# Kernel tuning notes

Measured on AMD Instinct MI355X. Metric: run time of the kernel, lower is better.

Reference implementation:

```python
import jax, jax.numpy as jnp
import numpy as np

MAXLEN = 100  # target_node_incoming_edge_maxlim in to_dense_batch_JY


def setup_inputs() -> dict:
    key = jax.random.key(0)
    ks = jax.random.split(key, 6)
    N, F, H, B = 500000, 64, 64, 8192
    x = jax.random.normal(ks[0], (N, F), dtype=jnp.float32)
    index = jnp.sort(jax.random.randint(ks[1], (N,), 0, B)).astype(jnp.int64)
    s = 1.0 / np.sqrt(H)  # torch LSTM reset_parameters: U(-1/sqrt(H), 1/sqrt(H))
    W_ih = jax.random.uniform(ks[2], (4 * H, F), jnp.float32, -s, s)
    W_hh = jax.random.uniform(ks[3], (4 * H, H), jnp.float32, -s, s)
    b_ih = jax.random.uniform(ks[4], (4 * H,), jnp.float32, -s, s)
    b_hh = jax.random.uniform(ks[5], (4 * H,), jnp.float32, -s, s)
    return {"x": x, "W_ih": W_ih, "W_hh": W_hh, "b_ih": b_ih, "b_hh": b_hh,
            "index": index, "dim_size": B}


def _lstm_last_hidden(dense, mask, W_ih, W_hh, b_ih, b_hh):
    """Run a single-layer LSTM over dense [B,L,F]; freeze state where mask is
    False, which reproduces pack_sequence semantics (ht = hidden at last valid
    step of each sequence; zero-length sequences stay at h0=0)."""
    B, L, F = dense.shape
    H = W_hh.shape[1]
    # input projection for all timesteps at once: [B, L, 4H]
    xg = jnp.einsum('blf,gf->blg', dense, W_ih) + (b_ih + b_hh)

    def step(carry, inp):
        h, c = carry
        g_x, m = inp                      # g_x: [B,4H], m: [B] bool
        g = g_x + h @ W_hh.T
        i, f, gc, o = jnp.split(g, 4, axis=-1)  # torch gate order: i, f, g, o
        i = jax.nn.sigmoid(i)
        f = jax.nn.sigmoid(f)
        gc = jnp.tanh(gc)
        o = jax.nn.sigmoid(o)
        c_new = f * c + i * gc
        h_new = o * jnp.tanh(c_new)
        m2 = m[:, None]
        return (jnp.where(m2, h_new, h), jnp.where(m2, c_new, c)), None

    h0 = jnp.zeros((B, H), dense.dtype)
    (h, _c), _ = jax.lax.scan(step, (h0, h0),
                              (jnp.swapaxes(xg, 0, 1), mask.T))
    return h  # [B, H] == ht[-1]


def reference(x, W_ih, W_hh, b_ih, b_hh, index, dim_size):
    N, F = x.shape
    index = index.astype(jnp.int32)
    # per-graph node counts and exclusive-cumsum offsets (index is sorted)
    counts = jax.ops.segment_sum(jnp.ones(N, jnp.int32), index,
                                 num_segments=dim_size)
    offsets = jnp.concatenate([jnp.zeros(1, jnp.int32),
                               jnp.cumsum(counts)[:-1].astype(jnp.int32)])
    pos = jnp.arange(N, dtype=jnp.int32) - offsets[index]  # position in graph
    valid = pos < MAXLEN                                   # truncate to 100
    # scatter into dense [B, MAXLEN, F]; invalid rows are zeroed and added at
    # slot 0 so they are no-ops
    dense = jnp.zeros((dim_size, MAXLEN, F), x.dtype)
    dense = dense.at[index, jnp.where(valid, pos, 0)].add(
        jnp.where(valid[:, None], x, 0.0))
    seq_len = jnp.minimum(counts, MAXLEN)
    mask = jnp.arange(MAXLEN)[None, :] < seq_len[:, None]  # [B, MAXLEN]
    return _lstm_last_hidden(dense, mask, W_ih, W_hh, b_ih, b_hh)
```

## Files before the change

kernel.cpp:

```cpp
#include <hip/hip_runtime.h>

#define MAXLEN 100
#define HDIM 64
#define CH 4
#define NSEG 12
#define SROW 72
#define SPLANE (CH * SROW + 8)
#define HSTR 72
#define L2E 1.44269504f

typedef __attribute__((ext_vector_type(8))) short bf16x8;
typedef __attribute__((ext_vector_type(4))) float f32x4;

#define LGKM_BARRIER() asm volatile("s_waitcnt lgkmcnt(0)\n\ts_barrier" ::: "memory")

__device__ __forceinline__ unsigned short f2bf_u(float f) {
    unsigned u = __float_as_uint(f);
    u += 0x7fffu + ((u >> 16) & 1u);
    return (unsigned short)(u >> 16);
}
__device__ __forceinline__ unsigned pk2(float a, float b) {
    return (unsigned)f2bf_u(a) | ((unsigned)f2bf_u(b) << 16);
}
__device__ __forceinline__ bf16x8 pack8(f32x4 a, f32x4 b) {
    union { unsigned u[4]; bf16x8 v; } c;
    c.u[0] = pk2(a[0], a[1]); c.u[1] = pk2(a[2], a[3]);
    c.u[2] = pk2(b[0], b[1]); c.u[3] = pk2(b[2], b[3]);
    return c.v;
}
__device__ __forceinline__ float sig_b(float v, float bs) {
    return __builtin_amdgcn_rcpf(1.0f + __builtin_amdgcn_exp2f(fmaf(v, -L2E, bs)));
}
__device__ __forceinline__ float tanh_b(float v, float bs2) {
    return fmaf(2.0f, __builtin_amdgcn_rcpf(1.0f + __builtin_amdgcn_exp2f(fmaf(v, -2.0f * L2E, bs2))), -1.0f);
}
__device__ __forceinline__ float tanh_p(float v) {
    return fmaf(2.0f, __builtin_amdgcn_rcpf(1.0f + __builtin_amdgcn_exp2f(v * (-2.0f * L2E))), -1.0f);
}

__global__ __launch_bounds__(256, 3)
void lstm12_kernel(const float* __restrict__ x,
                   const float* __restrict__ Wih,
                   const float* __restrict__ Whh,
                   const float* __restrict__ bih,
                   const float* __restrict__ bhh,
                   const int* __restrict__ index,
                   float* __restrict__ out, int N, int B) {
    const int tid  = threadIdx.x;
    const int w    = tid >> 6;
    const int lane = tid & 63;
    const int l15  = lane & 15;
    const int quad = lane >> 4;
    const int segbase = blockIdx.x * NSEG;
    const int ncol = w * 16 + l15;

    __shared__ __align__(16) unsigned short xst[NSEG * SPLANE];
    __shared__ __align__(16) unsigned short hst[2][16][HSTR];
    __shared__ int sstart[NSEG], slen[NSEG];

    if (tid < NSEG) {
        const int b = segbase + tid;
        int s = 0, len = 0;
        if (b < B) {
            int lo = 0, hi = N;
            while (lo < hi) { int m = (lo + hi) >> 1; if (index[m] < b) lo = m + 1; else hi = m; }
            s = lo;
            hi = N;
            while (lo < hi) { int m = (lo + hi) >> 1; if (index[m] < b + 1) lo = m + 1; else hi = m; }
            len = lo - s;
            len = len < MAXLEN ? len : MAXLEN;
        }
        sstart[tid] = s;
        slen[tid] = len;
    }
    for (int i = tid; i < 2 * 16 * HSTR / 2; i += 256) ((int*)hst)[i] = 0;
    __syncthreads();

    bf16x8 wi[4][2], wh[4][2];
    float bs[4];
#pragma unroll
    for (int g = 0; g < 4; ++g) {
        const int row = g * HDIM + ncol;
        const float bb = bih[row] + bhh[row];
        bs[g] = (g == 2) ? (-2.0f * L2E) * bb : (-L2E) * bb;
#pragma unroll
        for (int kt = 0; kt < 2; ++kt) {
            const f32x4* pi = (const f32x4*)(Wih + (size_t)row * HDIM + kt * 32 + quad * 8);
            const f32x4* ph = (const f32x4*)(Whh + (size_t)row * HDIM + kt * 32 + quad * 8);
            wi[g][kt] = pack8(pi[0], pi[1]);
            wh[g][kt] = pack8(ph[0], ph[1]);
        }
    }

    int len3[3];
#pragma unroll
    for (int r = 0; r < 3; ++r) len3[r] = slen[quad * 3 + r];
    int lmax = 0;
#pragma unroll
    for (int i = 0; i < NSEG; ++i) { int v = slen[i]; lmax = v > lmax ? v : lmax; }
    lmax = __builtin_amdgcn_readfirstlane(lmax);

    const int sS = tid >> 4, sT = (tid >> 2) & 3, sC = tid & 3;
    const int sst = (tid < 192) ? sstart[sS] : 0;
    const int sln = (tid < 192) ? slen[sS] : 0;

    f32x4 pre[4];

#define ISSUE(t0_)                                                              \
    if (w < 3) {                                                                \
        int ct = (t0_) + sT;                                                    \
        ct = (sln > 0) ? (ct < sln ? ct : sln - 1) : 0;                         \
        int row = sst + ct;                                                     \
        row = row < N - 1 ? row : N - 1;                                        \
        const f32x4* p_ = (const f32x4*)(x + (size_t)row * HDIM + sC * 16);     \
        pre[0] = p_[0]; pre[1] = p_[1]; pre[2] = p_[2]; pre[3] = p_[3];         \
    }
#define COMMIT()                                                                \
    if (w < 3) {                                                                \
        uint4 o1, o2;                                                           \
        o1.x = pk2(pre[0][0], pre[0][1]); o1.y = pk2(pre[0][2], pre[0][3]);     \
        o1.z = pk2(pre[1][0], pre[1][1]); o1.w = pk2(pre[1][2], pre[1][3]);     \
        o2.x = pk2(pre[2][0], pre[2][1]); o2.y = pk2(pre[2][2], pre[2][3]);     \
        o2.z = pk2(pre[3][0], pre[3][1]); o2.w = pk2(pre[3][2], pre[3][3]);     \
        unsigned short* d_ = &xst[sS * SPLANE + sT * SROW + sC * 16];           \
        *(uint4*)d_ = o1; *(uint4*)(d_ + 8) = o2;                               \
    }

    const int m3 = l15 & 3;
    const int xp = (l15 >> 2) * 3 + (m3 < 2 ? m3 : 2);
    const unsigned short* xb = &xst[xp * SPLANE + quad * 8];

    f32x4 accx[4];
#define ACCX(tt_)                                                               \
    {                                                                           \
        const unsigned short* xr_ = xb + (tt_) * SROW;                          \
        bf16x8 xa0_ = *(const bf16x8*)(xr_);                                    \
        bf16x8 xa1_ = *(const bf16x8*)(xr_ + 32);                               \
        _Pragma("unroll")                                                       \
        for (int g_ = 0; g_ < 4; ++g_) {                                        \
            f32x4 a_ = __builtin_amdgcn_mfma_f32_16x16x32_bf16(xa0_, wi[g_][0], cz, 0, 0, 0); \
            accx[g_] = __builtin_amdgcn_mfma_f32_16x16x32_bf16(xa1_, wi[g_][1], a_, 0, 0, 0); \
        }                                                                       \
    }

    float c3[3] = {0, 0, 0}, h3[3] = {0, 0, 0};
    const f32x4 cz = {0.0f, 0.0f, 0.0f, 0.0f};
    const int nch = (lmax + CH - 1) / CH;

    if (nch > 0) {
        ISSUE(0);
        COMMIT();
        LGKM_BARRIER();
        ACCX(0);
        if (nch > 1) ISSUE(CH);

        for (int ch = 0; ch < nch; ++ch) {
            const int t0 = ch * CH;
#pragma unroll
            for (int tt = 0; tt < CH; ++tt) {
                const int t = t0 + tt;
                const int pb = tt & 1, nb = pb ^ 1;

                const unsigned short* hr = &hst[pb][l15][quad * 8];
                bf16x8 ha0 = *(const bf16x8*)(hr);
                bf16x8 ha1 = *(const bf16x8*)(hr + 32);

                f32x4 acc[4];
#pragma unroll
                for (int g = 0; g < 4; ++g) {
                    f32x4 a = __builtin_amdgcn_mfma_f32_16x16x32_bf16(ha0, wh[g][0], accx[g], 0, 0, 0);
                    acc[g] = __builtin_amdgcn_mfma_f32_16x16x32_bf16(ha1, wh[g][1], a, 0, 0, 0);
                }

                if (tt + 1 < CH) ACCX(tt + 1);

#pragma unroll
                for (int r = 0; r < 3; ++r) {
                    float gi = sig_b (acc[0][r], bs[0]);
                    float gf = sig_b (acc[1][r], bs[1]);
                    float gg = tanh_b(acc[2][r], bs[2]);
                    float go = sig_b (acc[3][r], bs[3]);
                    float cn = fmaf(gf, c3[r], gi * gg);
                    float hn = go * tanh_p(cn);
                    const bool up = t < len3[r];
                    c3[r] = up ? cn : c3[r];
                    h3[r] = up ? hn : h3[r];
                    hst[nb][quad * 4 + r][ncol] = f2bf_u(h3[r]);
                }
                LGKM_BARRIER();
            }
            if (ch + 1 < nch) {
                COMMIT();
                LGKM_BARRIER();
                ACCX(0);
                if (ch + 2 < nch) ISSUE((ch + 2) * CH);
            }
        }
    }

#pragma unroll
    for (int r = 0; r < 3; ++r) {
        const int seg = segbase + quad * 3 + r;
        if (seg < B) out[(size_t)seg * HDIM + ncol] = h3[r];
    }
#undef ISSUE
#undef COMMIT
#undef ACCX
}

extern "C" void kernel_launch(void* const* d_in, const int* in_sizes, int n_in,
                              void* d_out, int out_size, void* d_ws, size_t ws_size,
                              hipStream_t stream) {
    const float* x     = (const float*)d_in[0];
    const float* Wih   = (const float*)d_in[1];
    const float* Whh   = (const float*)d_in[2];
    const float* bih   = (const float*)d_in[3];
    const float* bhh   = (const float*)d_in[4];
    const int*   index = (const int*)d_in[5];

    const int N = in_sizes[5];
    const int B = out_size / HDIM;

    const int nblocks = (B + NSEG - 1) / NSEG;
    lstm12_kernel<<<nblocks, 256, 0, stream>>>(x, Wih, Whh, bih, bhh, index,
                                               (float*)d_out, N, B);
}
```

Baseline: 251.5 us.

## Run each LSTM group in a single wave with all weights in registers

Replaces the 256-thread, 12-segment block with a single 64-lane wave that handles 8 segments and holds all four gate column tiles of W_ih and W_hh in registers. This removes the cross-wave barriers and the LDS staging of x, since x rows are loaded straight into registers two steps ahead. The gate scale factors are folded into the weights, the bias seeds the MFMA accumulator, and bf16 conversion uses the hardware v_cvt_pk_bf16_f32 instruction. In exchange each wave does four times the MFMA work per step on a serial dependency chain, register pressure rises sharply, and the MFMA tiles use only 8 of their 16 rows.

```diff
diff --git a/kernel.cpp b/kernel.cpp
--- a/kernel.cpp
+++ b/kernel.cpp
@@ -2,210 +2,163 @@
 
 #define MAXLEN 100
 #define HDIM 64
-#define CH 4
-#define NSEG 12
-#define SROW 72
-#define SPLANE (CH * SROW + 8)
+#define SEGW 8
 #define HSTR 72
 #define L2E 1.44269504f
 
 typedef __attribute__((ext_vector_type(8))) short bf16x8;
 typedef __attribute__((ext_vector_type(4))) float f32x4;
 
-#define LGKM_BARRIER() asm volatile("s_waitcnt lgkmcnt(0)\n\ts_barrier" ::: "memory")
-
-__device__ __forceinline__ unsigned short f2bf_u(float f) {
-    unsigned u = __float_as_uint(f);
-    u += 0x7fffu + ((u >> 16) & 1u);
-    return (unsigned short)(u >> 16);
-}
-__device__ __forceinline__ unsigned pk2(float a, float b) {
-    return (unsigned)f2bf_u(a) | ((unsigned)f2bf_u(b) << 16);
+__device__ __forceinline__ unsigned cvtpk(float a, float b) {
+    unsigned r;
+    asm("v_cvt_pk_bf16_f32 %0, %1, %2" : "=v"(r) : "v"(a), "v"(b));
+    return r;
 }
 __device__ __forceinline__ bf16x8 pack8(f32x4 a, f32x4 b) {
     union { unsigned u[4]; bf16x8 v; } c;
-    c.u[0] = pk2(a[0], a[1]); c.u[1] = pk2(a[2], a[3]);
-    c.u[2] = pk2(b[0], b[1]); c.u[3] = pk2(b[2], b[3]);
+    c.u[0] = cvtpk(a[0], a[1]); c.u[1] = cvtpk(a[2], a[3]);
+    c.u[2] = cvtpk(b[0], b[1]); c.u[3] = cvtpk(b[2], b[3]);
     return c.v;
 }
-__device__ __forceinline__ float sig_b(float v, float bs) {
-    return __builtin_amdgcn_rcpf(1.0f + __builtin_amdgcn_exp2f(fmaf(v, -L2E, bs)));
+__device__ __forceinline__ float sig_pre(float a) {
+    return __builtin_amdgcn_rcpf(1.0f + __builtin_amdgcn_exp2f(a));
 }
-__device__ __forceinline__ float tanh_b(float v, float bs2) {
-    return fmaf(2.0f, __builtin_amdgcn_rcpf(1.0f + __builtin_amdgcn_exp2f(fmaf(v, -2.0f * L2E, bs2))), -1.0f);
+__device__ __forceinline__ float tanh_pre(float a) {
+    return fmaf(2.0f, __builtin_amdgcn_rcpf(1.0f + __builtin_amdgcn_exp2f(a)), -1.0f);
 }
 __device__ __forceinline__ float tanh_p(float v) {
     return fmaf(2.0f, __builtin_amdgcn_rcpf(1.0f + __builtin_amdgcn_exp2f(v * (-2.0f * L2E))), -1.0f);
 }
 
-__global__ __launch_bounds__(256, 3)
-void lstm12_kernel(const float* __restrict__ x,
-                   const float* __restrict__ Wih,
-                   const float* __restrict__ Whh,
-                   const float* __restrict__ bih,
-                   const float* __restrict__ bhh,
-                   const int* __restrict__ index,
-                   float* __restrict__ out, int N, int B) {
-    const int tid  = threadIdx.x;
-    const int w    = tid >> 6;
-    const int lane = tid & 63;
+__global__ __launch_bounds__(64, 1)
+void lstm_wave_kernel(const float* __restrict__ x,
+                      const float* __restrict__ Wih,
+                      const float* __restrict__ Whh,
+                      const float* __restrict__ bih,
+                      const float* __restrict__ bhh,
+                      const int* __restrict__ index,
+                      float* __restrict__ out, int N, int B) {
+    const int lane = threadIdx.x;
     const int l15  = lane & 15;
     const int quad = lane >> 4;
-    const int segbase = blockIdx.x * NSEG;
-    const int ncol = w * 16 + l15;
+    const int segbase = blockIdx.x * SEGW;
 
-    __shared__ __align__(16) unsigned short xst[NSEG * SPLANE];
-    __shared__ __align__(16) unsigned short hst[2][16][HSTR];
-    __shared__ int sstart[NSEG], slen[NSEG];
+    __shared__ __align__(16) unsigned short hlds[SEGW * HSTR];
+    __shared__ int sb[SEGW + 1];
 
-    if (tid < NSEG) {
-        const int b = segbase + tid;
-        int s = 0, len = 0;
-        if (b < B) {
-            int lo = 0, hi = N;
-            while (lo < hi) { int m = (lo + hi) >> 1; if (index[m] < b) lo = m + 1; else hi = m; }
-            s = lo;
-            hi = N;
-            while (lo < hi) { int m = (lo + hi) >> 1; if (index[m] < b + 1) lo = m + 1; else hi = m; }
-            len = lo - s;
-            len = len < MAXLEN ? len : MAXLEN;
-        }
-        sstart[tid] = s;
-        slen[tid] = len;
+    if (lane <= SEGW) {
+        int tgt = segbase + lane; tgt = tgt < B ? tgt : B;
+        int lo = 0, hi = N;
+        while (lo < hi) { int m = (lo + hi) >> 1; if (index[m] < tgt) lo = m + 1; else hi = m; }
+        sb[lane] = lo;
     }
-    for (int i = tid; i < 2 * 16 * HSTR / 2; i += 256) ((int*)hst)[i] = 0;
+    for (int i = lane; i < SEGW * HSTR / 2; i += 64) ((int*)hlds)[i] = 0;
     __syncthreads();
 
-    bf16x8 wi[4][2], wh[4][2];
-    float bs[4];
+    bf16x8 wi[4][4][2], wh[4][4][2];
+    float bsv[4][4];
 #pragma unroll
     for (int g = 0; g < 4; ++g) {
-        const int row = g * HDIM + ncol;
-        const float bb = bih[row] + bhh[row];
-        bs[g] = (g == 2) ? (-2.0f * L2E) * bb : (-L2E) * bb;
+        const float sc = (g == 2) ? (-2.0f * L2E) : (-L2E);
 #pragma unroll
-        for (int kt = 0; kt < 2; ++kt) {
-            const f32x4* pi = (const f32x4*)(Wih + (size_t)row * HDIM + kt * 32 + quad * 8);
-            const f32x4* ph = (const f32x4*)(Whh + (size_t)row * HDIM + kt * 32 + quad * 8);
-            wi[g][kt] = pack8(pi[0], pi[1]);
-            wh[g][kt] = pack8(ph[0], ph[1]);
-        }
-    }
-
-    int len3[3];
+        for (int ct = 0; ct < 4; ++ct) {
+            const int row = g * HDIM + ct * 16 + l15;
+            bsv[g][ct] = sc * (bih[row] + bhh[row]);
 #pragma unroll
-    for (int r = 0; r < 3; ++r) len3[r] = slen[quad * 3 + r];
-    int lmax = 0;
-#pragma unroll
-    for (int i = 0; i < NSEG; ++i) { int v = slen[i]; lmax = v > lmax ? v : lmax; }
-    lmax = __builtin_amdgcn_readfirstlane(lmax);
-
-    const int sS = tid >> 4, sT = (tid >> 2) & 3, sC = tid & 3;
-    const int sst = (tid < 192) ? sstart[sS] : 0;
-    const int sln = (tid < 192) ? slen[sS] : 0;
-
-    f32x4 pre[4];
-
-#define ISSUE(t0_)                                                              \
-    if (w < 3) {                                                                \
-        int ct = (t0_) + sT;                                                    \
-        ct = (sln > 0) ? (ct < sln ? ct : sln - 1) : 0;                         \
-        int row = sst + ct;                                                     \
-        row = row < N - 1 ? row : N - 1;                                        \
-        const f32x4* p_ = (const f32x4*)(x + (size_t)row * HDIM + sC * 16);     \
-        pre[0] = p_[0]; pre[1] = p_[1]; pre[2] = p_[2]; pre[3] = p_[3];         \
-    }
-#define COMMIT()                                                                \
-    if (w < 3) {                                                                \
-        uint4 o1, o2;                                                           \
-        o1.x = pk2(pre[0][0], pre[0][1]); o1.y = pk2(pre[0][2], pre[0][3]);     \
-        o1.z = pk2(pre[1][0], pre[1][1]); o1.w = pk2(pre[1][2], pre[1][3]);     \
-        o2.x = pk2(pre[2][0], pre[2][1]); o2.y = pk2(pre[2][2], pre[2][3]);     \
-        o2.z = pk2(pre[3][0], pre[3][1]); o2.w = pk2(pre[3][2], pre[3][3]);     \
-        unsigned short* d_ = &xst[sS * SPLANE + sT * SROW + sC * 16];           \
-        *(uint4*)d_ = o1; *(uint4*)(d_ + 8) = o2;                               \
-    }
-
-    const int m3 = l15 & 3;
-    const int xp = (l15 >> 2) * 3 + (m3 < 2 ? m3 : 2);
-    const unsigned short* xb = &xst[xp * SPLANE + quad * 8];
-
-    f32x4 accx[4];
-#define ACCX(tt_)                                                               \
-    {                                                                           \
-        const unsigned short* xr_ = xb + (tt_) * SROW;                          \
-        bf16x8 xa0_ = *(const bf16x8*)(xr_);                                    \
-        bf16x8 xa1_ = *(const bf16x8*)(xr_ + 32);                               \
-        _Pragma("unroll")                                                       \
-        for (int g_ = 0; g_ < 4; ++g_) {                                        \
-            f32x4 a_ = __builtin_amdgcn_mfma_f32_16x16x32_bf16(xa0_, wi[g_][0], cz, 0, 0, 0); \
-            accx[g_] = __builtin_amdgcn_mfma_f32_16x16x32_bf16(xa1_, wi[g_][1], a_, 0, 0, 0); \
-        }                                                                       \
-    }
-
-    float c3[3] = {0, 0, 0}, h3[3] = {0, 0, 0};
-    const f32x4 cz = {0.0f, 0.0f, 0.0f, 0.0f};
-    const int nch = (lmax + CH - 1) / CH;
-
-    if (nch > 0) {
-        ISSUE(0);
-        COMMIT();
-        LGKM_BARRIER();
-        ACCX(0);
-        if (nch > 1) ISSUE(CH);
-
-        for (int ch = 0; ch < nch; ++ch) {
-            const int t0 = ch * CH;
-#pragma unroll
-            for (int tt = 0; tt < CH; ++tt) {
-                const int t = t0 + tt;
-                const int pb = tt & 1, nb = pb ^ 1;
-
-                const unsigned short* hr = &hst[pb][l15][quad * 8];
-                bf16x8 ha0 = *(const bf16x8*)(hr);
-                bf16x8 ha1 = *(const bf16x8*)(hr + 32);
-
-                f32x4 acc[4];
-#pragma unroll
-                for (int g = 0; g < 4; ++g) {
-                    f32x4 a = __builtin_amdgcn_mfma_f32_16x16x32_bf16(ha0, wh[g][0], accx[g], 0, 0, 0);
-                    acc[g] = __builtin_amdgcn_mfma_f32_16x16x32_bf16(ha1, wh[g][1], a, 0, 0, 0);
-                }
-
-                if (tt + 1 < CH) ACCX(tt + 1);
-
-#pragma unroll
-                for (int r = 0; r < 3; ++r) {
-                    float gi = sig_b (acc[0][r], bs[0]);
-                    float gf = sig_b (acc[1][r], bs[1]);
-                    float gg = tanh_b(acc[2][r], bs[2]);
-                    float go = sig_b (acc[3][r], bs[3]);
-                    float cn = fmaf(gf, c3[r], gi * gg);
-                    float hn = go * tanh_p(cn);
-                    const bool up = t < len3[r];
-                    c3[r] = up ? cn : c3[r];
-                    h3[r] = up ? hn : h3[r];
-                    hst[nb][quad * 4 + r][ncol] = f2bf_u(h3[r]);
-                }
-                LGKM_BARRIER();
-            }
-            if (ch + 1 < nch) {
-                COMMIT();
-                LGKM_BARRIER();
-                ACCX(0);
-                if (ch + 2 < nch) ISSUE((ch + 2) * CH);
+            for (int kt = 0; kt < 2; ++kt) {
+                const f32x4* pi = (const f32x4*)(Wih + (size_t)row * HDIM + kt * 32 + quad * 8);
+                const f32x4* ph = (const f32x4*)(Whh + (size_t)row * HDIM + kt * 32 + quad * 8);
+                wi[g][ct][kt] = pack8(pi[0] * sc, pi[1] * sc);
+                wh[g][ct][kt] = pack8(ph[0] * sc, ph[1] * sc);
             }
         }
     }
 
+    const int sA   = ((l15 >> 2) << 1) | (l15 & 1);
+    const int sstA = sb[sA];
+    int lenA = sb[sA + 1] - sstA; lenA = lenA < MAXLEN ? lenA : MAXLEN;
+
+    int len2[2];
 #pragma unroll
-    for (int r = 0; r < 3; ++r) {
-        const int seg = segbase + quad * 3 + r;
-        if (seg < B) out[(size_t)seg * HDIM + ncol] = h3[r];
+    for (int r = 0; r < 2; ++r) {
+        const int s = quad * 2 + r;
+        int l = sb[s + 1] - sb[s];
+        len2[r] = l < MAXLEN ? l : MAXLEN;
     }
-#undef ISSUE
-#undef COMMIT
-#undef ACCX
+    int lmax = 0;
+#pragma unroll
+    for (int i = 0; i < SEGW; ++i) {
+        int l = sb[i + 1] - sb[i]; l = l < MAXLEN ? l : MAXLEN;
+        lmax = l > lmax ? l : lmax;
+    }
+    lmax = __builtin_amdgcn_readfirstlane(lmax);
+
+    f32x4 pfA[4], pfB[4];
+#define XLOAD(PF_, T_) {                                                        \
+        int ct_ = (T_); ct_ = lenA > 0 ? (ct_ < lenA ? ct_ : lenA - 1) : 0;     \
+        int row_ = sstA + ct_; row_ = row_ < N - 1 ? row_ : N - 1;              \
+        const f32x4* p_ = (const f32x4*)(x + (size_t)row_ * HDIM + quad * 8);   \
+        PF_[0] = p_[0]; PF_[1] = p_[1];                                         \
+        const f32x4* q_ = (const f32x4*)(x + (size_t)row_ * HDIM + 32 + quad * 8); \
+        PF_[2] = q_[0]; PF_[3] = q_[1]; }
+
+    float c2[4][2] = {{0, 0}, {0, 0}, {0, 0}, {0, 0}};
+    float h2[4][2] = {{0, 0}, {0, 0}, {0, 0}, {0, 0}};
+
+#define STEP(T_, PF_) {                                                         \
+        const int t_ = (T_);                                                    \
+        bf16x8 xa0 = pack8(PF_[0], PF_[1]);                                     \
+        bf16x8 xa1 = pack8(PF_[2], PF_[3]);                                     \
+        bf16x8 ha0 = *(const bf16x8*)(hlds + sA * HSTR + quad * 8);             \
+        bf16x8 ha1 = *(const bf16x8*)(hlds + sA * HSTR + 32 + quad * 8);        \
+        XLOAD(PF_, t_ + 2);                                                     \
+        f32x4 acc[4][4];                                                        \
+        _Pragma("unroll") for (int g = 0; g < 4; ++g)                           \
+        _Pragma("unroll") for (int ct = 0; ct < 4; ++ct) {                      \
+            f32x4 seed = {bsv[g][ct], bsv[g][ct], bsv[g][ct], bsv[g][ct]};      \
+            f32x4 a_ = __builtin_amdgcn_mfma_f32_16x16x32_bf16(xa0, wi[g][ct][0], seed, 0, 0, 0); \
+            acc[g][ct] = __builtin_amdgcn_mfma_f32_16x16x32_bf16(xa1, wi[g][ct][1], a_, 0, 0, 0); \
+        }                                                                       \
+        _Pragma("unroll") for (int g = 0; g < 4; ++g)                           \
+        _Pragma("unroll") for (int ct = 0; ct < 4; ++ct) {                      \
+            f32x4 a_ = __builtin_amdgcn_mfma_f32_16x16x32_bf16(ha0, wh[g][ct][0], acc[g][ct], 0, 0, 0); \
+            acc[g][ct] = __builtin_amdgcn_mfma_f32_16x16x32_bf16(ha1, wh[g][ct][1], a_, 0, 0, 0); \
+        }                                                                       \
+        _Pragma("unroll") for (int ct = 0; ct < 4; ++ct)                        \
+        _Pragma("unroll") for (int r = 0; r < 2; ++r) {                         \
+            float gi = sig_pre (acc[0][ct][r]);                                 \
+            float gf = sig_pre (acc[1][ct][r]);                                 \
+            float gg = tanh_pre(acc[2][ct][r]);                                 \
+            float go = sig_pre (acc[3][ct][r]);                                 \
+            float cn = fmaf(gf, c2[ct][r], gi * gg);                            \
+            float hn = go * tanh_p(cn);                                         \
+            const bool up = t_ < len2[r];                                       \
+            c2[ct][r] = up ? cn : c2[ct][r];                                    \
+            h2[ct][r] = up ? hn : h2[ct][r];                                    \
+            hlds[(quad * 2 + r) * HSTR + ct * 16 + l15] =                       \
+                (unsigned short)cvtpk(h2[ct][r], h2[ct][r]);                    \
+        } }
+
+    if (lmax > 0) {
+        XLOAD(pfA, 0);
+        XLOAD(pfB, 1);
+        for (int t = 0; t < lmax; t += 2) {
+            STEP(t, pfA);
+            if (t + 1 < lmax) STEP(t + 1, pfB);
+        }
+    }
+
+#pragma unroll
+    for (int r = 0; r < 2; ++r) {
+        const int seg = segbase + quad * 2 + r;
+        if (seg < B) {
+#pragma unroll
+            for (int ct = 0; ct < 4; ++ct)
+                out[(size_t)seg * HDIM + ct * 16 + l15] = h2[ct][r];
+        }
+    }
+#undef XLOAD
+#undef STEP
 }
 
 extern "C" void kernel_launch(void* const* d_in, const int* in_sizes, int n_in,
@@ -221,7 +174,7 @@
     const int N = in_sizes[5];
     const int B = out_size / HDIM;
 
-    const int nblocks = (B + NSEG - 1) / NSEG;
-    lstm12_kernel<<<nblocks, 256, 0, stream>>>(x, Wih, Whh, bih, bhh, index,
-                                               (float*)d_out, N, B);
+    const int nblocks = (B + SEGW - 1) / SEGW;
+    lstm_wave_kernel<<<nblocks, 64, 0, stream>>>(x, Wih, Whh, bih, bhh, index,
+                                                 (float*)d_out, N, B);
 }
```

Result: slower. 316.0 us (+25.7%).
